# Optimization experiments

Measured on AMD Instinct MI355X. Metric: run time of the kernel, lower is better.

Reference implementation:

```python
import jax, jax.numpy as jnp
import numpy as np

N_HEAD = 16
N_FEAT = 1024
D_HEAD = N_FEAT // N_HEAD


def setup_inputs() -> dict:
    key = jax.random.key(0)
    ks = jax.random.split(key, 12)
    B, L, T = 8, 128, 64
    s = 0.05
    return {
        "q": jax.random.normal(ks[0], (B, 1, N_FEAT), jnp.float32),
        "kv": jax.random.normal(ks[1], (B, L, T, N_FEAT), jnp.float32),
        "Wq": jax.random.normal(ks[2], (D_HEAD, D_HEAD), jnp.float32) * s,
        "bq": jax.random.normal(ks[3], (D_HEAD,), jnp.float32) * s,
        "Wk": jax.random.normal(ks[4], (D_HEAD, D_HEAD), jnp.float32) * s,
        "bk": jax.random.normal(ks[5], (D_HEAD,), jnp.float32) * s,
        "Wv": jax.random.normal(ks[6], (D_HEAD, D_HEAD), jnp.float32) * s,
        "bv": jax.random.normal(ks[7], (D_HEAD,), jnp.float32) * s,
        "Wo": jax.random.normal(ks[8], (N_FEAT, N_FEAT), jnp.float32) * s,
        "bo": jax.random.normal(ks[9], (N_FEAT,), jnp.float32) * s,
    }


def reference(q, kv, Wq, bq, Wk, bk, Wv, bv, Wo, bo):
    B, L, T, D = kv.shape
    H, dh = N_HEAD, D_HEAD
    # mean-pool q over its singleton length dim and kv over T for keys
    qm = q.mean(axis=-2)                      # [B, D]
    km = kv.mean(axis=-2)                     # [B, L, D]
    qh = qm.reshape(B, H, dh)                 # [B, H, dh]
    kh = km.reshape(B, L, H, dh)              # [B, L, H, dh]
    vh = kv.reshape(B, L, T, H, dh)           # [B, L, T, H, dh]
    # per-head linear projections (torch Linear: x @ W.T + b)
    qh = qh @ Wq.T + bq
    kh = kh @ Wk.T + bk
    vh = vh @ Wv.T + bv
    # faithful transpose chain from the original module
    qh = jnp.swapaxes(qh, -2, -3)             # [H, B, dh]  (3D: swaps B and H)
    kh = jnp.swapaxes(kh, -2, -3)             # [B, H, L, dh]
    # broadcasted matmul -> cross-batch attention [B, H, B, L]
    attw = jnp.matmul(qh, jnp.swapaxes(kh, -1, -2)) / jnp.sqrt(jnp.float32(dh))
    attn = jax.nn.softmax(attw, axis=-1)      # [B, H, B, L]
    # value reshuffle: [B,L,T,H,dh] -> [B,H,T,L,dh] -> [B,H,T,dh,L] -> [B,H,T*dh,L]
    v = jnp.swapaxes(vh, -2, -4)
    v = jnp.swapaxes(v, -1, -2)
    v = v.reshape(B, H, T * dh, L)
    ct = jnp.matmul(attn, jnp.swapaxes(v, -1, -2))   # [B, H, B, T*dh]
    ct = ct.reshape(B, H, B, T, dh)
    ct = jnp.swapaxes(ct, -2, -4)                    # [B, T, B, H, dh]
    ct = ct.reshape(B, T, B, H * dh)                 # [B, T, B, D]
    return ct @ Wo.T + bo
```

## Files before the change

kernel.cpp:

```cpp
#include <hip/hip_runtime.h>
#include <hip/hip_bf16.h>

#define BDIM 8
#define LDIM 128
#define TDIM 64
#define NFEAT 1024
#define HNUM 16
#define DH 64

#define GM 4096
#define GN 1024
#define GK 1024

typedef __attribute__((ext_vector_type(8))) short short8;
typedef __attribute__((ext_vector_type(4))) float f32x4;

__device__ __forceinline__ unsigned short f2bf(float x) {
  union { float f; unsigned u; } v; v.f = x;
  unsigned r = v.u + 0x7fffu + ((v.u >> 16) & 1u);
  return (unsigned short)(r >> 16);
}

__device__ __forceinline__ void gload_lds16(const void* g, void* l) {
  __builtin_amdgcn_global_load_lds((const __attribute__((address_space(1))) void*)g,
                                   (__attribute__((address_space(3))) void*)l, 16, 0, 0);
}

__global__ __launch_bounds__(256) void mean_kernel(const float* __restrict__ kv,
                                                   float* __restrict__ km) {
  const int bl = blockIdx.x;
  const float* src = kv + (size_t)bl * (TDIM * NFEAT) + threadIdx.x * 4;
  float4 acc = make_float4(0.f, 0.f, 0.f, 0.f);
  for (int t0 = 0; t0 < TDIM; t0 += 8) {
    float4 v[8];
#pragma unroll
    for (int j = 0; j < 8; ++j) v[j] = *(const float4*)(src + (t0 + j) * NFEAT);
#pragma unroll
    for (int j = 0; j < 8; ++j) {
      acc.x += v[j].x; acc.y += v[j].y; acc.z += v[j].z; acc.w += v[j].w;
    }
  }
  const float s = 1.f / TDIM;
  const float4 o = make_float4(acc.x * s, acc.y * s, acc.z * s, acc.w * s);
  *(float4*)(km + (size_t)bl * NFEAT + threadIdx.x * 4) = o;
}

__global__ __launch_bounds__(128) void attn_kernel(const float* __restrict__ q,
                                                   const float* __restrict__ km,
                                                   const float* __restrict__ Wq,
                                                   const float* __restrict__ bq,
                                                   const float* __restrict__ Wk,
                                                   float* __restrict__ attn) {
  __shared__ float qp_s[BDIM * DH];
  __shared__ float qk_s[BDIM * DH];
  __shared__ float sw[BDIM * LDIM];
  __shared__ float mred[BDIM], ired[BDIM];
  const int b1 = blockIdx.x;
  const int h  = blockIdx.y;
  const int tid = threadIdx.x;

  {
    const int e0 = tid * 4;
    const int b2 = e0 >> 6;
    const int d0 = e0 & 63;
    float a0 = bq[d0], a1 = bq[d0 + 1], a2 = bq[d0 + 2], a3 = bq[d0 + 3];
    const float* qrow = q + b2 * NFEAT + h * DH;
#pragma unroll 4
    for (int i = 0; i < DH; ++i) {
      const float qv = qrow[i];
      a0 += qv * Wq[(d0 + 0) * DH + i];
      a1 += qv * Wq[(d0 + 1) * DH + i];
      a2 += qv * Wq[(d0 + 2) * DH + i];
      a3 += qv * Wq[(d0 + 3) * DH + i];
    }
    qp_s[e0 + 0] = a0; qp_s[e0 + 1] = a1; qp_s[e0 + 2] = a2; qp_s[e0 + 3] = a3;
  }
  __syncthreads();
  {
    const int e0 = tid * 4;
    const int b2 = e0 >> 6;
    const int i0 = e0 & 63;
    float a0 = 0, a1 = 0, a2 = 0, a3 = 0;
#pragma unroll 4
    for (int d = 0; d < DH; ++d) {
      const float qpv = qp_s[b2 * DH + d];
      const float4 wk4 = *(const float4*)(Wk + d * DH + i0);
      a0 += qpv * wk4.x; a1 += qpv * wk4.y; a2 += qpv * wk4.z; a3 += qpv * wk4.w;
    }
    qk_s[e0 + 0] = a0; qk_s[e0 + 1] = a1; qk_s[e0 + 2] = a2; qk_s[e0 + 3] = a3;
  }
  __syncthreads();
  const int l = tid;
  {
    const float* kmrow = km + (size_t)(b1 * LDIM + l) * NFEAT + h * DH;
    float s[8] = {0, 0, 0, 0, 0, 0, 0, 0};
#pragma unroll
    for (int i4 = 0; i4 < DH / 4; ++i4) {
      const float4 kmv = *(const float4*)(kmrow + i4 * 4);
#pragma unroll
      for (int b2 = 0; b2 < 8; ++b2) {
        const float4 qk4 = *(const float4*)(qk_s + b2 * DH + i4 * 4);
        s[b2] += kmv.x * qk4.x + kmv.y * qk4.y + kmv.z * qk4.z + kmv.w * qk4.w;
      }
    }
#pragma unroll
    for (int b2 = 0; b2 < 8; ++b2) sw[b2 * LDIM + l] = s[b2] * 0.125f;
  }
  __syncthreads();
  if (tid < 8) {
    const int b2 = tid;
    float m = -1e30f;
    for (int j = 0; j < LDIM; ++j) m = fmaxf(m, sw[b2 * LDIM + j]);
    float ssum = 0.f;
    for (int j = 0; j < LDIM; ++j) ssum += expf(sw[b2 * LDIM + j] - m);
    mred[b2] = m;
    ired[b2] = 1.f / ssum;
  }
  __syncthreads();
  float* abase = attn + ((size_t)(b1 * HNUM + h) * BDIM) * LDIM + l;
#pragma unroll
  for (int b2 = 0; b2 < 8; ++b2) {
    abase[b2 * LDIM] = expf(sw[b2 * LDIM + l] - mred[b2]) * ired[b2];
  }
}

__global__ __launch_bounds__(256) void weff_kernel(const float* __restrict__ Wo,
                                                   const float* __restrict__ Wv,
                                                   const float* __restrict__ bv,
                                                   const float* __restrict__ bo,
                                                   unsigned short* __restrict__ Weff,
                                                   float* __restrict__ beff) {
  __shared__ float worow[NFEAT];
  __shared__ float red[256];
  const int f = blockIdx.x;
  const int tid = threadIdx.x;
  *(float4*)(worow + tid * 4) = *(const float4*)(Wo + (size_t)f * NFEAT + tid * 4);
  __syncthreads();
  const int g0 = tid * 4;
  const int hbase = (g0 >> 6) << 6;
  const int i0 = g0 & 63;
  float a0 = 0, a1 = 0, a2 = 0, a3 = 0;
#pragma unroll 4
  for (int d = 0; d < DH; ++d) {
    const float wod = worow[hbase + d];
    const float4 wv4 = *(const float4*)(Wv + d * DH + i0);
    a0 += wod * wv4.x; a1 += wod * wv4.y; a2 += wod * wv4.z; a3 += wod * wv4.w;
  }
  ushort4 pk;
  pk.x = f2bf(a0); pk.y = f2bf(a1); pk.z = f2bf(a2); pk.w = f2bf(a3);
  *(ushort4*)(Weff + (size_t)f * NFEAT + g0) = pk;
  red[tid] = worow[g0 + 0] * bv[i0 + 0] + worow[g0 + 1] * bv[i0 + 1] +
             worow[g0 + 2] * bv[i0 + 2] + worow[g0 + 3] * bv[i0 + 3];
  __syncthreads();
  for (int sft = 128; sft > 0; sft >>= 1) {
    if (tid < sft) red[tid] += red[tid + sft];
    __syncthreads();
  }
  if (tid == 0) beff[f] = bo[f] + red[0];
}

#define HSTRIDE 1032
__global__ __launch_bounds__(64) void pool_kernel(const float* __restrict__ kv,
                                                  const float* __restrict__ attn,
                                                  unsigned short* __restrict__ pooled) {
  __shared__ float wlds[4 * HSTRIDE];
  const int b1 = blockIdx.x;
  const int t = blockIdx.y;
  const int ftile = blockIdx.z;
  const int tid = threadIdx.x;
  {
#pragma unroll
    for (int hg = 0; hg < 4; ++hg) {
      const float* src = attn + ((size_t)(b1 * HNUM + ftile * 4 + hg)) * (BDIM * LDIM);
#pragma unroll
      for (int j = 0; j < 4; ++j) {
        const int idx = (j * 64 + tid) * 4;
        *(float4*)(wlds + hg * HSTRIDE + idx) = *(const float4*)(src + idx);
      }
    }
  }
  __syncthreads();
  const int f = ftile * 256 + tid * 4;
  const int hh = tid >> 4;
  const float* kvbase = kv + ((size_t)b1 * LDIM) * (TDIM * NFEAT) + t * NFEAT + f;
  float4 acc[8];
#pragma unroll
  for (int b2 = 0; b2 < 8; ++b2) acc[b2] = make_float4(0.f, 0.f, 0.f, 0.f);
  const float* wbase = wlds + hh * HSTRIDE;
  for (int l0 = 0; l0 < LDIM; l0 += 8) {
    float4 v[8];
#pragma unroll
    for (int j = 0; j < 8; ++j)
      v[j] = *(const float4*)(kvbase + (size_t)(l0 + j) * (TDIM * NFEAT));
#pragma unroll
    for (int j = 0; j < 8; ++j) {
#pragma unroll
      for (int b2 = 0; b2 < 8; ++b2) {
        const float w = wbase[b2 * LDIM + l0 + j];
        acc[b2].x += w * v[j].x; acc[b2].y += w * v[j].y;
        acc[b2].z += w * v[j].z; acc[b2].w += w * v[j].w;
      }
    }
  }
  unsigned short* obase = pooled + ((size_t)(b1 * TDIM + t) * BDIM) * NFEAT + f;
#pragma unroll
  for (int b2 = 0; b2 < 8; ++b2) {
    ushort4 pk;
    pk.x = f2bf(acc[b2].x); pk.y = f2bf(acc[b2].y);
    pk.z = f2bf(acc[b2].z); pk.w = f2bf(acc[b2].w);
    *(ushort4*)(obase + b2 * NFEAT) = pk;
  }
}

__global__ __launch_bounds__(256) void mfma_gemm(const unsigned short* __restrict__ A,
                                                 const unsigned short* __restrict__ W,
                                                 const float* __restrict__ beff,
                                                 float* __restrict__ out) {
  __shared__ unsigned short As[2][128 * 32];
  __shared__ unsigned short Bs[2][64 * 32];
  const int tid = threadIdx.x;
  const int w = tid >> 6, l = tid & 63;
  const int mBase = blockIdx.y * 128, nBase = blockIdx.x * 64;
  const int wr = w >> 1, wc = w & 1;

  int arow[2], acol[2];
#pragma unroll
  for (int j = 0; j < 2; ++j) {
    const int cid = j * 256 + tid;
    const int r = cid >> 2, c = cid & 3;
    arow[j] = r;
    acol[j] = (c ^ ((r >> 1) & 3)) * 8;
  }
  const int brow = tid >> 2;
  const int bcol = ((tid & 3) ^ ((brow >> 1) & 3)) * 8;

  const int rl = l & 15, ks = l >> 4;
  const int fsel = (ks ^ ((rl >> 1) & 3)) * 16;

  f32x4 acc[4][2] = {};

#pragma unroll
  for (int j = 0; j < 2; ++j)
    gload_lds16(A + (size_t)(mBase + arow[j]) * GK + acol[j],
                (char*)As[0] + (j * 256 + tid) * 16);
  gload_lds16(W + (size_t)(nBase + brow) * GK + bcol, (char*)Bs[0] + tid * 16);
  __syncthreads();

  int cur = 0;
  for (int t = 0; t < GK / 32; ++t) {
    if (t + 1 < GK / 32) {
      const int k0 = (t + 1) * 32;
#pragma unroll
      for (int j = 0; j < 2; ++j)
        gload_lds16(A + (size_t)(mBase + arow[j]) * GK + k0 + acol[j],
                    (char*)As[cur ^ 1] + (j * 256 + tid) * 16);
      gload_lds16(W + (size_t)(nBase + brow) * GK + k0 + bcol,
                  (char*)Bs[cur ^ 1] + tid * 16);
    }
    short8 a[4], b[2];
#pragma unroll
    for (int m = 0; m < 4; ++m)
      a[m] = *(const short8*)((const char*)As[cur] + (wr * 64 + m * 16 + rl) * 64 + fsel);
#pragma unroll
    for (int n = 0; n < 2; ++n)
      b[n] = *(const short8*)((const char*)Bs[cur] + (wc * 32 + n * 16 + rl) * 64 + fsel);
#pragma unroll
    for (int m = 0; m < 4; ++m)
#pragma unroll
      for (int n = 0; n < 2; ++n)
        acc[m][n] = __builtin_amdgcn_mfma_f32_16x16x32_bf16(a[m], b[n], acc[m][n], 0, 0, 0);
    __syncthreads();
    cur ^= 1;
  }

#pragma unroll
  for (int n = 0; n < 2; ++n) {
    const int col = nBase + wc * 32 + n * 16 + rl;
    const float bv = beff[col];
#pragma unroll
    for (int m = 0; m < 4; ++m) {
      const int row0 = mBase + wr * 64 + m * 16 + ks * 4;
#pragma unroll
      for (int j2 = 0; j2 < 4; ++j2)
        out[(size_t)(row0 + j2) * GN + col] = acc[m][n][j2] + bv;
    }
  }
}

extern "C" void kernel_launch(void* const* d_in, const int* in_sizes, int n_in,
                              void* d_out, int out_size, void* d_ws, size_t ws_size,
                              hipStream_t stream) {
  const float* q  = (const float*)d_in[0];
  const float* kv = (const float*)d_in[1];
  const float* Wq = (const float*)d_in[2];
  const float* bq = (const float*)d_in[3];
  const float* Wk = (const float*)d_in[4];
  const float* Wv = (const float*)d_in[6];
  const float* bv = (const float*)d_in[7];
  const float* Wo = (const float*)d_in[8];
  const float* bo = (const float*)d_in[9];
  float* out = (float*)d_out;

  char* ws = (char*)d_ws;
  float*          km     = (float*)ws;
  float*          attn   = (float*)(ws + (4u << 20));
  float*          beff   = (float*)(ws + (4u << 20) + (512u << 10));
  unsigned short* Weff   = (unsigned short*)(ws + (4u << 20) + (516u << 10));
  unsigned short* pooled = (unsigned short*)(ws + (4u << 20) + (516u << 10) + (2u << 20));

  weff_kernel<<<NFEAT, 256, 0, stream>>>(Wo, Wv, bv, bo, Weff, beff);
  mean_kernel<<<BDIM * LDIM, 256, 0, stream>>>(kv, km);
  attn_kernel<<<dim3(BDIM, HNUM), 128, 0, stream>>>(q, km, Wq, bq, Wk, attn);
  pool_kernel<<<dim3(BDIM, TDIM, 4), 64, 0, stream>>>(kv, attn, pooled);
  mfma_gemm<<<dim3(GN / 64, GM / 128), 256, 0, stream>>>(pooled, Weff, beff, out);
}
```

Baseline: 147.9 us.

## Fuse all five stages into one cooperative persistent kernel with grid syncs

Replaces the five separate launches (weight fold, mean, attention, pooling, GEMM) with a single cooperative kernel of 256 blocks that runs each stage in turn, separated by grid-wide syncs. The pooling stage is remapped so each block handles two (b1,t) units for all 1024 features, with the attention weights transposed into LDS so each weight load serves all heads. The goal is to remove per-launch overhead and tail gaps between small kernels. In exchange, each stage is limited to 256 blocks of 256 threads, which lowers occupancy and parallelism for the bandwidth-bound mean and pool stages, and the grid syncs add their own cost.

Measured after the change: 247.6 us. 67.4% more time.

```diff
diff --git a/kernel.cpp b/kernel.cpp
--- a/kernel.cpp
+++ b/kernel.cpp
@@ -1,5 +1,8 @@
 #include <hip/hip_runtime.h>
 #include <hip/hip_bf16.h>
+#include <hip/hip_cooperative_groups.h>
+
+namespace cg = cooperative_groups;
 
 #define BDIM 8
 #define LDIM 128
@@ -26,263 +29,275 @@
                                    (__attribute__((address_space(3))) void*)l, 16, 0, 0);
 }
 
-__global__ __launch_bounds__(256) void mean_kernel(const float* __restrict__ kv,
-                                                   float* __restrict__ km) {
-  const int bl = blockIdx.x;
-  const float* src = kv + (size_t)bl * (TDIM * NFEAT) + threadIdx.x * 4;
-  float4 acc = make_float4(0.f, 0.f, 0.f, 0.f);
-  for (int t0 = 0; t0 < TDIM; t0 += 8) {
-    float4 v[8];
-#pragma unroll
-    for (int j = 0; j < 8; ++j) v[j] = *(const float4*)(src + (t0 + j) * NFEAT);
-#pragma unroll
-    for (int j = 0; j < 8; ++j) {
-      acc.x += v[j].x; acc.y += v[j].y; acc.z += v[j].z; acc.w += v[j].w;
-    }
-  }
-  const float s = 1.f / TDIM;
-  const float4 o = make_float4(acc.x * s, acc.y * s, acc.z * s, acc.w * s);
-  *(float4*)(km + (size_t)bl * NFEAT + threadIdx.x * 4) = o;
-}
-
-__global__ __launch_bounds__(128) void attn_kernel(const float* __restrict__ q,
-                                                   const float* __restrict__ km,
-                                                   const float* __restrict__ Wq,
-                                                   const float* __restrict__ bq,
-                                                   const float* __restrict__ Wk,
-                                                   float* __restrict__ attn) {
-  __shared__ float qp_s[BDIM * DH];
-  __shared__ float qk_s[BDIM * DH];
-  __shared__ float sw[BDIM * LDIM];
-  __shared__ float mred[BDIM], ired[BDIM];
-  const int b1 = blockIdx.x;
-  const int h  = blockIdx.y;
+__global__ __launch_bounds__(256) void fused_kernel(
+    const float* __restrict__ q, const float* __restrict__ kv,
+    const float* __restrict__ Wq, const float* __restrict__ bq,
+    const float* __restrict__ Wk, const float* __restrict__ Wv,
+    const float* __restrict__ bv, const float* __restrict__ Wo,
+    const float* __restrict__ bo, float* __restrict__ km,
+    float* __restrict__ attnW, unsigned short* __restrict__ Weff,
+    float* __restrict__ beff, unsigned short* __restrict__ pooled,
+    float* __restrict__ out) {
+  __shared__ char smem_raw[65536];
+  float* smf = (float*)smem_raw;
   const int tid = threadIdx.x;
-
-  {
-    const int e0 = tid * 4;
-    const int b2 = e0 >> 6;
-    const int d0 = e0 & 63;
-    float a0 = bq[d0], a1 = bq[d0 + 1], a2 = bq[d0 + 2], a3 = bq[d0 + 3];
-    const float* qrow = q + b2 * NFEAT + h * DH;
+  const int blk = blockIdx.x;
+  cg::grid_group grid = cg::this_grid();
+
+  {
+#pragma unroll
+    for (int j = 0; j < 4; ++j) {
+      const int bl = blk * 4 + j;
+      const float* src = kv + (size_t)bl * (TDIM * NFEAT) + tid * 4;
+      float4 acc = make_float4(0.f, 0.f, 0.f, 0.f);
+      for (int t0 = 0; t0 < TDIM; t0 += 8) {
+        float4 v[8];
+#pragma unroll
+        for (int jj = 0; jj < 8; ++jj)
+          v[jj] = *(const float4*)(src + (t0 + jj) * NFEAT);
+#pragma unroll
+        for (int jj = 0; jj < 8; ++jj) {
+          acc.x += v[jj].x; acc.y += v[jj].y; acc.z += v[jj].z; acc.w += v[jj].w;
+        }
+      }
+      const float s = 1.f / TDIM;
+      const float4 o = make_float4(acc.x * s, acc.y * s, acc.z * s, acc.w * s);
+      *(float4*)(km + (size_t)bl * NFEAT + tid * 4) = o;
+    }
+  }
+  {
+    float* worow = smf;
+    float* red   = smf + 1024;
+    for (int j = 0; j < 4; ++j) {
+      const int f = blk * 4 + j;
+      *(float4*)(worow + tid * 4) = *(const float4*)(Wo + (size_t)f * NFEAT + tid * 4);
+      __syncthreads();
+      const int g0 = tid * 4;
+      const int hbase = (g0 >> 6) << 6;
+      const int i0 = g0 & 63;
+      float a0 = 0, a1 = 0, a2 = 0, a3 = 0;
 #pragma unroll 4
-    for (int i = 0; i < DH; ++i) {
-      const float qv = qrow[i];
-      a0 += qv * Wq[(d0 + 0) * DH + i];
-      a1 += qv * Wq[(d0 + 1) * DH + i];
-      a2 += qv * Wq[(d0 + 2) * DH + i];
-      a3 += qv * Wq[(d0 + 3) * DH + i];
-    }
-    qp_s[e0 + 0] = a0; qp_s[e0 + 1] = a1; qp_s[e0 + 2] = a2; qp_s[e0 + 3] = a3;
-  }
-  __syncthreads();
-  {
-    const int e0 = tid * 4;
-    const int b2 = e0 >> 6;
-    const int i0 = e0 & 63;
-    float a0 = 0, a1 = 0, a2 = 0, a3 = 0;
+      for (int d = 0; d < DH; ++d) {
+        const float wod = worow[hbase + d];
+        const float4 wv4 = *(const float4*)(Wv + d * DH + i0);
+        a0 += wod * wv4.x; a1 += wod * wv4.y; a2 += wod * wv4.z; a3 += wod * wv4.w;
+      }
+      ushort4 pk;
+      pk.x = f2bf(a0); pk.y = f2bf(a1); pk.z = f2bf(a2); pk.w = f2bf(a3);
+      *(ushort4*)(Weff + (size_t)f * NFEAT + g0) = pk;
+      red[tid] = worow[g0 + 0] * bv[i0 + 0] + worow[g0 + 1] * bv[i0 + 1] +
+                 worow[g0 + 2] * bv[i0 + 2] + worow[g0 + 3] * bv[i0 + 3];
+      __syncthreads();
+      for (int sft = 128; sft > 0; sft >>= 1) {
+        if (tid < sft) red[tid] += red[tid + sft];
+        __syncthreads();
+      }
+      if (tid == 0) beff[f] = bo[f] + red[0];
+    }
+  }
+  grid.sync();
+
+  {
+    float* qp_s = smf;
+    float* qk_s = smf + 512;
+    float* sw   = smf + 1024;
+    float* mred = smf + 2048;
+    float* ired = smf + 2056;
+    const int b1 = blk >> 4;
+    const int h  = blk & 15;
+    const bool act = (blk < 128) && (tid < 128);
+    if (act) {
+      const int e0 = tid * 4;
+      const int b2 = e0 >> 6;
+      const int d0 = e0 & 63;
+      float a0 = bq[d0], a1 = bq[d0 + 1], a2 = bq[d0 + 2], a3 = bq[d0 + 3];
+      const float* qrow = q + b2 * NFEAT + h * DH;
 #pragma unroll 4
-    for (int d = 0; d < DH; ++d) {
-      const float qpv = qp_s[b2 * DH + d];
-      const float4 wk4 = *(const float4*)(Wk + d * DH + i0);
-      a0 += qpv * wk4.x; a1 += qpv * wk4.y; a2 += qpv * wk4.z; a3 += qpv * wk4.w;
-    }
-    qk_s[e0 + 0] = a0; qk_s[e0 + 1] = a1; qk_s[e0 + 2] = a2; qk_s[e0 + 3] = a3;
-  }
-  __syncthreads();
-  const int l = tid;
-  {
-    const float* kmrow = km + (size_t)(b1 * LDIM + l) * NFEAT + h * DH;
-    float s[8] = {0, 0, 0, 0, 0, 0, 0, 0};
-#pragma unroll
-    for (int i4 = 0; i4 < DH / 4; ++i4) {
-      const float4 kmv = *(const float4*)(kmrow + i4 * 4);
+      for (int i = 0; i < DH; ++i) {
+        const float qv = qrow[i];
+        a0 += qv * Wq[(d0 + 0) * DH + i];
+        a1 += qv * Wq[(d0 + 1) * DH + i];
+        a2 += qv * Wq[(d0 + 2) * DH + i];
+        a3 += qv * Wq[(d0 + 3) * DH + i];
+      }
+      qp_s[e0 + 0] = a0; qp_s[e0 + 1] = a1; qp_s[e0 + 2] = a2; qp_s[e0 + 3] = a3;
+    }
+    __syncthreads();
+    if (act) {
+      const int e0 = tid * 4;
+      const int b2 = e0 >> 6;
+      const int i0 = e0 & 63;
+      float a0 = 0, a1 = 0, a2 = 0, a3 = 0;
+#pragma unroll 4
+      for (int d = 0; d < DH; ++d) {
+        const float qpv = qp_s[b2 * DH + d];
+        const float4 wk4 = *(const float4*)(Wk + d * DH + i0);
+        a0 += qpv * wk4.x; a1 += qpv * wk4.y; a2 += qpv * wk4.z; a3 += qpv * wk4.w;
+      }
+      qk_s[e0 + 0] = a0; qk_s[e0 + 1] = a1; qk_s[e0 + 2] = a2; qk_s[e0 + 3] = a3;
+    }
+    __syncthreads();
+    if (act) {
+      const int l = tid;
+      const float* kmrow = km + (size_t)(b1 * LDIM + l) * NFEAT + h * DH;
+      float s[8] = {0, 0, 0, 0, 0, 0, 0, 0};
+#pragma unroll
+      for (int i4 = 0; i4 < DH / 4; ++i4) {
+        const float4 kmv = *(const float4*)(kmrow + i4 * 4);
+#pragma unroll
+        for (int b2 = 0; b2 < 8; ++b2) {
+          const float4 qk4 = *(const float4*)(qk_s + b2 * DH + i4 * 4);
+          s[b2] += kmv.x * qk4.x + kmv.y * qk4.y + kmv.z * qk4.z + kmv.w * qk4.w;
+        }
+      }
+#pragma unroll
+      for (int b2 = 0; b2 < 8; ++b2) sw[b2 * LDIM + tid] = s[b2] * 0.125f;
+    }
+    __syncthreads();
+    if (act && tid < 8) {
+      const int b2 = tid;
+      float m = -1e30f;
+      for (int j = 0; j < LDIM; ++j) m = fmaxf(m, sw[b2 * LDIM + j]);
+      float ssum = 0.f;
+      for (int j = 0; j < LDIM; ++j) ssum += expf(sw[b2 * LDIM + j] - m);
+      mred[b2] = m;
+      ired[b2] = 1.f / ssum;
+    }
+    __syncthreads();
+    if (act) {
+      float* abase = attnW + ((size_t)(b1 * HNUM + h) * BDIM) * LDIM + tid;
+#pragma unroll
+      for (int b2 = 0; b2 < 8; ++b2)
+        abase[b2 * LDIM] = expf(sw[b2 * LDIM + tid] - mred[b2]) * ired[b2];
+    }
+  }
+  grid.sync();
+
+  {
+    float* alds = smf;
+    const int u0 = blk * 2;
+    const int pb1 = u0 >> 6;
+#pragma unroll
+    for (int j = 0; j < 16; ++j) {
+      const int fl = j * 256 + tid;
+      const int l4 = fl & 31;
+      const int b2 = (fl >> 5) & 7;
+      const int h  = fl >> 8;
+      const float4 a4 = *(const float4*)(attnW +
+          ((size_t)(pb1 * HNUM + h) * BDIM + b2) * LDIM + l4 * 4);
+      alds[((l4 * 4 + 0) * 8 + b2) * 16 + h] = a4.x;
+      alds[((l4 * 4 + 1) * 8 + b2) * 16 + h] = a4.y;
+      alds[((l4 * 4 + 2) * 8 + b2) * 16 + h] = a4.z;
+      alds[((l4 * 4 + 3) * 8 + b2) * 16 + h] = a4.w;
+    }
+    __syncthreads();
+    const int f0 = tid * 4;
+    const int h = tid >> 4;
+    for (int j = 0; j < 2; ++j) {
+      const int u = u0 + j;
+      const int t = u & 63;
+      const float* kvb = kv + (((size_t)pb1 * LDIM) * TDIM + t) * NFEAT + f0;
+      float4 acc[8];
+#pragma unroll
+      for (int b2 = 0; b2 < 8; ++b2) acc[b2] = make_float4(0.f, 0.f, 0.f, 0.f);
+      for (int l0 = 0; l0 < LDIM; l0 += 8) {
+        float4 v[8];
+#pragma unroll
+        for (int jj = 0; jj < 8; ++jj)
+          v[jj] = *(const float4*)(kvb + (size_t)(l0 + jj) * (TDIM * NFEAT));
+#pragma unroll
+        for (int jj = 0; jj < 8; ++jj) {
+#pragma unroll
+          for (int b2 = 0; b2 < 8; ++b2) {
+            const float w = alds[((l0 + jj) * 8 + b2) * 16 + h];
+            acc[b2].x += w * v[jj].x; acc[b2].y += w * v[jj].y;
+            acc[b2].z += w * v[jj].z; acc[b2].w += w * v[jj].w;
+          }
+        }
+      }
+      unsigned short* obase = pooled + ((size_t)u * BDIM) * NFEAT + f0;
 #pragma unroll
       for (int b2 = 0; b2 < 8; ++b2) {
-        const float4 qk4 = *(const float4*)(qk_s + b2 * DH + i4 * 4);
-        s[b2] += kmv.x * qk4.x + kmv.y * qk4.y + kmv.z * qk4.z + kmv.w * qk4.w;
-      }
-    }
-#pragma unroll
-    for (int b2 = 0; b2 < 8; ++b2) sw[b2 * LDIM + l] = s[b2] * 0.125f;
-  }
-  __syncthreads();
-  if (tid < 8) {
-    const int b2 = tid;
-    float m = -1e30f;
-    for (int j = 0; j < LDIM; ++j) m = fmaxf(m, sw[b2 * LDIM + j]);
-    float ssum = 0.f;
-    for (int j = 0; j < LDIM; ++j) ssum += expf(sw[b2 * LDIM + j] - m);
-    mred[b2] = m;
-    ired[b2] = 1.f / ssum;
-  }
-  __syncthreads();
-  float* abase = attn + ((size_t)(b1 * HNUM + h) * BDIM) * LDIM + l;
-#pragma unroll
-  for (int b2 = 0; b2 < 8; ++b2) {
-    abase[b2 * LDIM] = expf(sw[b2 * LDIM + l] - mred[b2]) * ired[b2];
-  }
-}
-
-__global__ __launch_bounds__(256) void weff_kernel(const float* __restrict__ Wo,
-                                                   const float* __restrict__ Wv,
-                                                   const float* __restrict__ bv,
-                                                   const float* __restrict__ bo,
-                                                   unsigned short* __restrict__ Weff,
-                                                   float* __restrict__ beff) {
-  __shared__ float worow[NFEAT];
-  __shared__ float red[256];
-  const int f = blockIdx.x;
-  const int tid = threadIdx.x;
-  *(float4*)(worow + tid * 4) = *(const float4*)(Wo + (size_t)f * NFEAT + tid * 4);
-  __syncthreads();
-  const int g0 = tid * 4;
-  const int hbase = (g0 >> 6) << 6;
-  const int i0 = g0 & 63;
-  float a0 = 0, a1 = 0, a2 = 0, a3 = 0;
-#pragma unroll 4
-  for (int d = 0; d < DH; ++d) {
-    const float wod = worow[hbase + d];
-    const float4 wv4 = *(const float4*)(Wv + d * DH + i0);
-    a0 += wod * wv4.x; a1 += wod * wv4.y; a2 += wod * wv4.z; a3 += wod * wv4.w;
-  }
-  ushort4 pk;
-  pk.x = f2bf(a0); pk.y = f2bf(a1); pk.z = f2bf(a2); pk.w = f2bf(a3);
-  *(ushort4*)(Weff + (size_t)f * NFEAT + g0) = pk;
-  red[tid] = worow[g0 + 0] * bv[i0 + 0] + worow[g0 + 1] * bv[i0 + 1] +
-             worow[g0 + 2] * bv[i0 + 2] + worow[g0 + 3] * bv[i0 + 3];
-  __syncthreads();
-  for (int sft = 128; sft > 0; sft >>= 1) {
-    if (tid < sft) red[tid] += red[tid + sft];
-    __syncthreads();
-  }
-  if (tid == 0) beff[f] = bo[f] + red[0];
-}
-
-#define HSTRIDE 1032
-__global__ __launch_bounds__(64) void pool_kernel(const float* __restrict__ kv,
-                                                  const float* __restrict__ attn,
-                                                  unsigned short* __restrict__ pooled) {
-  __shared__ float wlds[4 * HSTRIDE];
-  const int b1 = blockIdx.x;
-  const int t = blockIdx.y;
-  const int ftile = blockIdx.z;
-  const int tid = threadIdx.x;
-  {
-#pragma unroll
-    for (int hg = 0; hg < 4; ++hg) {
-      const float* src = attn + ((size_t)(b1 * HNUM + ftile * 4 + hg)) * (BDIM * LDIM);
-#pragma unroll
-      for (int j = 0; j < 4; ++j) {
-        const int idx = (j * 64 + tid) * 4;
-        *(float4*)(wlds + hg * HSTRIDE + idx) = *(const float4*)(src + idx);
-      }
-    }
-  }
-  __syncthreads();
-  const int f = ftile * 256 + tid * 4;
-  const int hh = tid >> 4;
-  const float* kvbase = kv + ((size_t)b1 * LDIM) * (TDIM * NFEAT) + t * NFEAT + f;
-  float4 acc[8];
-#pragma unroll
-  for (int b2 = 0; b2 < 8; ++b2) acc[b2] = make_float4(0.f, 0.f, 0.f, 0.f);
-  const float* wbase = wlds + hh * HSTRIDE;
-  for (int l0 = 0; l0 < LDIM; l0 += 8) {
-    float4 v[8];
-#pragma unroll
-    for (int j = 0; j < 8; ++j)
-      v[j] = *(const float4*)(kvbase + (size_t)(l0 + j) * (TDIM * NFEAT));
-#pragma unroll
-    for (int j = 0; j < 8; ++j) {
-#pragma unroll
-      for (int b2 = 0; b2 < 8; ++b2) {
-        const float w = wbase[b2 * LDIM + l0 + j];
-        acc[b2].x += w * v[j].x; acc[b2].y += w * v[j].y;
-        acc[b2].z += w * v[j].z; acc[b2].w += w * v[j].w;
-      }
-    }
-  }
-  unsigned short* obase = pooled + ((size_t)(b1 * TDIM + t) * BDIM) * NFEAT + f;
-#pragma unroll
-  for (int b2 = 0; b2 < 8; ++b2) {
-    ushort4 pk;
-    pk.x = f2bf(acc[b2].x); pk.y = f2bf(acc[b2].y);
-    pk.z = f2bf(acc[b2].z); pk.w = f2bf(acc[b2].w);
-    *(ushort4*)(obase + b2 * NFEAT) = pk;
-  }
-}
-
-__global__ __launch_bounds__(256) void mfma_gemm(const unsigned short* __restrict__ A,
-                                                 const unsigned short* __restrict__ W,
-                                                 const float* __restrict__ beff,
-                                                 float* __restrict__ out) {
-  __shared__ unsigned short As[2][128 * 32];
-  __shared__ unsigned short Bs[2][64 * 32];
-  const int tid = threadIdx.x;
-  const int w = tid >> 6, l = tid & 63;
-  const int mBase = blockIdx.y * 128, nBase = blockIdx.x * 64;
-  const int wr = w >> 1, wc = w & 1;
-
-  int arow[2], acol[2];
-#pragma unroll
-  for (int j = 0; j < 2; ++j) {
-    const int cid = j * 256 + tid;
-    const int r = cid >> 2, c = cid & 3;
-    arow[j] = r;
-    acol[j] = (c ^ ((r >> 1) & 3)) * 8;
-  }
-  const int brow = tid >> 2;
-  const int bcol = ((tid & 3) ^ ((brow >> 1) & 3)) * 8;
-
-  const int rl = l & 15, ks = l >> 4;
-  const int fsel = (ks ^ ((rl >> 1) & 3)) * 16;
-
-  f32x4 acc[4][2] = {};
-
-#pragma unroll
-  for (int j = 0; j < 2; ++j)
-    gload_lds16(A + (size_t)(mBase + arow[j]) * GK + acol[j],
-                (char*)As[0] + (j * 256 + tid) * 16);
-  gload_lds16(W + (size_t)(nBase + brow) * GK + bcol, (char*)Bs[0] + tid * 16);
-  __syncthreads();
-
-  int cur = 0;
-  for (int t = 0; t < GK / 32; ++t) {
-    if (t + 1 < GK / 32) {
-      const int k0 = (t + 1) * 32;
+        ushort4 pk;
+        pk.x = f2bf(acc[b2].x); pk.y = f2bf(acc[b2].y);
+        pk.z = f2bf(acc[b2].z); pk.w = f2bf(acc[b2].w);
+        *(ushort4*)(obase + b2 * NFEAT) = pk;
+      }
+    }
+  }
+  grid.sync();
+
+  {
+    unsigned short* As = (unsigned short*)smem_raw;
+    unsigned short* Bs = (unsigned short*)(smem_raw + 16384);
+    const unsigned short* A = pooled;
+    const unsigned short* W = Weff;
+    const int w = tid >> 6, l = tid & 63;
+    const int wr = w >> 1, wc = w & 1;
+    int arow[2], acol[2];
+#pragma unroll
+    for (int j = 0; j < 2; ++j) {
+      const int cid = j * 256 + tid;
+      const int r = cid >> 2, c = cid & 3;
+      arow[j] = r;
+      acol[j] = (c ^ ((r >> 1) & 3)) * 8;
+    }
+    const int brow = tid >> 2;
+    const int bcol = ((tid & 3) ^ ((brow >> 1) & 3)) * 8;
+    const int rl = l & 15, ks = l >> 4;
+    const int fsel = (ks ^ ((rl >> 1) & 3)) * 16;
+
+    for (int tile = blk * 2; tile < blk * 2 + 2; ++tile) {
+      const int mBase = (tile >> 4) * 128;
+      const int nBase = (tile & 15) * 64;
+      f32x4 acc[4][2] = {};
 #pragma unroll
       for (int j = 0; j < 2; ++j)
-        gload_lds16(A + (size_t)(mBase + arow[j]) * GK + k0 + acol[j],
-                    (char*)As[cur ^ 1] + (j * 256 + tid) * 16);
-      gload_lds16(W + (size_t)(nBase + brow) * GK + k0 + bcol,
-                  (char*)Bs[cur ^ 1] + tid * 16);
-    }
-    short8 a[4], b[2];
-#pragma unroll
-    for (int m = 0; m < 4; ++m)
-      a[m] = *(const short8*)((const char*)As[cur] + (wr * 64 + m * 16 + rl) * 64 + fsel);
-#pragma unroll
-    for (int n = 0; n < 2; ++n)
-      b[n] = *(const short8*)((const char*)Bs[cur] + (wc * 32 + n * 16 + rl) * 64 + fsel);
-#pragma unroll
-    for (int m = 0; m < 4; ++m)
-#pragma unroll
-      for (int n = 0; n < 2; ++n)
-        acc[m][n] = __builtin_amdgcn_mfma_f32_16x16x32_bf16(a[m], b[n], acc[m][n], 0, 0, 0);
-    __syncthreads();
-    cur ^= 1;
-  }
-
-#pragma unroll
-  for (int n = 0; n < 2; ++n) {
-    const int col = nBase + wc * 32 + n * 16 + rl;
-    const float bv = beff[col];
-#pragma unroll
-    for (int m = 0; m < 4; ++m) {
-      const int row0 = mBase + wr * 64 + m * 16 + ks * 4;
-#pragma unroll
-      for (int j2 = 0; j2 < 4; ++j2)
-        out[(size_t)(row0 + j2) * GN + col] = acc[m][n][j2] + bv;
+        gload_lds16(A + (size_t)(mBase + arow[j]) * GK + acol[j],
+                    (char*)As + (j * 256 + tid) * 16);
+      gload_lds16(W + (size_t)(nBase + brow) * GK + bcol, (char*)Bs + tid * 16);
+      __syncthreads();
+      int cur = 0;
+      for (int t = 0; t < GK / 32; ++t) {
+        if (t + 1 < GK / 32) {
+          const int k0 = (t + 1) * 32;
+#pragma unroll
+          for (int j = 0; j < 2; ++j)
+            gload_lds16(A + (size_t)(mBase + arow[j]) * GK + k0 + acol[j],
+                        (char*)(As + (cur ^ 1) * 4096) + (j * 256 + tid) * 16);
+          gload_lds16(W + (size_t)(nBase + brow) * GK + k0 + bcol,
+                      (char*)(Bs + (cur ^ 1) * 2048) + tid * 16);
+        }
+        short8 a[4], b[2];
+#pragma unroll
+        for (int m = 0; m < 4; ++m)
+          a[m] = *(const short8*)((const char*)(As + cur * 4096) +
+                                  (wr * 64 + m * 16 + rl) * 64 + fsel);
+#pragma unroll
+        for (int n = 0; n < 2; ++n)
+          b[n] = *(const short8*)((const char*)(Bs + cur * 2048) +
+                                  (wc * 32 + n * 16 + rl) * 64 + fsel);
+#pragma unroll
+        for (int m = 0; m < 4; ++m)
+#pragma unroll
+          for (int n = 0; n < 2; ++n)
+            acc[m][n] = __builtin_amdgcn_mfma_f32_16x16x32_bf16(a[m], b[n], acc[m][n], 0, 0, 0);
+        __syncthreads();
+        cur ^= 1;
+      }
+#pragma unroll
+      for (int n = 0; n < 2; ++n) {
+        const int col = nBase + wc * 32 + n * 16 + rl;
+        const float bvv = beff[col];
+#pragma unroll
+        for (int m = 0; m < 4; ++m) {
+          const int row0 = mBase + wr * 64 + m * 16 + ks * 4;
+#pragma unroll
+          for (int j2 = 0; j2 < 4; ++j2)
+            out[(size_t)(row0 + j2) * GN + col] = acc[m][n][j2] + bvv;
+        }
+      }
+      __syncthreads();
     }
   }
 }
@@ -303,14 +318,15 @@
 
   char* ws = (char*)d_ws;
   float*          km     = (float*)ws;
-  float*          attn   = (float*)(ws + (4u << 20));
+  float*          attnW  = (float*)(ws + (4u << 20));
   float*          beff   = (float*)(ws + (4u << 20) + (512u << 10));
   unsigned short* Weff   = (unsigned short*)(ws + (4u << 20) + (516u << 10));
   unsigned short* pooled = (unsigned short*)(ws + (4u << 20) + (516u << 10) + (2u << 20));
 
-  weff_kernel<<<NFEAT, 256, 0, stream>>>(Wo, Wv, bv, bo, Weff, beff);
-  mean_kernel<<<BDIM * LDIM, 256, 0, stream>>>(kv, km);
-  attn_kernel<<<dim3(BDIM, HNUM), 128, 0, stream>>>(q, km, Wq, bq, Wk, attn);
-  pool_kernel<<<dim3(BDIM, TDIM, 4), 64, 0, stream>>>(kv, attn, pooled);
-  mfma_gemm<<<dim3(GN / 64, GM / 128), 256, 0, stream>>>(pooled, Weff, beff, out);
+  void* args[] = {(void*)&q,  (void*)&kv, (void*)&Wq,   (void*)&bq,
+                  (void*)&Wk, (void*)&Wv, (void*)&bv,   (void*)&Wo,
+                  (void*)&bo, (void*)&km, (void*)&attnW,(void*)&Weff,
+                  (void*)&beff, (void*)&pooled, (void*)&out};
+  hipLaunchCooperativeKernel((void*)fused_kernel, dim3(256), dim3(256),
+                             args, 0, stream);
 }
```
